# Optimization experiments

Hardware: AMD Instinct MI355X
Metric: run time of the kernel (lower is better)

The kernel has to match this reference:

```python
import jax, jax.numpy as jnp
import numpy as np

EPS = 1e-5
B, L, E, H, F, HW = 32, 6, 3, 3, 2048, 32

def _ln(x, g, b):
    mu = jnp.mean(x, -1, keepdims=True)
    v = jnp.mean((x - mu) ** 2, -1, keepdims=True)
    return (x - mu) / jnp.sqrt(v + EPS) * g + b

def setup_inputs() -> dict:
    key = jax.random.key(0)
    ks = jax.random.split(key, 16)
    s = 0.05
    return {
        "x": jax.random.normal(ks[0], (B, 3, HW, HW), jnp.float32),
        "conv_w": jax.random.normal(ks[1], (3, 1, HW, HW), jnp.float32) * s,
        "conv_b": jax.random.normal(ks[2], (3,), jnp.float32) * s,
        "Wqkv": jax.random.normal(ks[3], (L, 3 * E, E), jnp.float32) * s,
        "bqkv": jax.random.normal(ks[4], (L, 3 * E), jnp.float32) * s,
        "Wo": jax.random.normal(ks[5], (L, E, E), jnp.float32) * s,
        "bo": jax.random.normal(ks[6], (L, E), jnp.float32) * s,
        "W1": jax.random.normal(ks[7], (L, F, E), jnp.float32) * s,
        "b1": jax.random.normal(ks[8], (L, F), jnp.float32) * s,
        "W2": jax.random.normal(ks[9], (L, E, F), jnp.float32) * s,
        "b2": jax.random.normal(ks[10], (L, E), jnp.float32) * s,
        "ln1_g": jnp.ones((L, E), jnp.float32),
        "ln1_b": jnp.zeros((L, E), jnp.float32),
        "ln2_g": jnp.ones((L, E), jnp.float32),
        "ln2_b": jnp.zeros((L, E), jnp.float32),
        "mlp_W": jax.random.normal(ks[11], (10, 3 * HW * HW), jnp.float32) * s,
        "mlp_b": jax.random.normal(ks[12], (10,), jnp.float32) * s,
    }

def reference(x, conv_w, conv_b, Wqkv, bqkv, Wo, bo, W1, b1, W2, b2,
              ln1_g, ln1_b, ln2_g, ln2_b, mlp_W, mlp_b):
    b = x.shape[0]
    # grouped conv with full-image kernel -> one scalar per channel
    c = jnp.einsum('bchw,chw->bc', x, conv_w[:, 0]) + conv_b  # (B,3)
    h = x + c[:, :, None, None]                               # residual add (broadcast)
    h = h.reshape(b, HW, HW, E)  # torch resize(32,32,3): raw memory reinterpret -> (B,S,N,E)
    for l in range(L):
        Wq, Wk, Wv = Wqkv[l, :E], Wqkv[l, E:2 * E], Wqkv[l, 2 * E:]
        bq, bk, bv = bqkv[l, :E], bqkv[l, E:2 * E], bqkv[l, 2 * E:]
        # head_dim = 1, so the feature axis doubles as the head axis
        q = (jnp.einsum('bsne,fe->bsnf', h, Wq) + bq)[..., None]  # (B,S,N,H,1)
        k = (jnp.einsum('bsne,fe->bsnf', h, Wk) + bk)[..., None]
        v = (jnp.einsum('bsne,fe->bsnf', h, Wv) + bv)[..., None]
        # scale = 1/sqrt(head_dim) = 1
        scores = jnp.einsum('bsnhd,btnhd->bnhst', q, k)
        attn = jax.nn.softmax(scores, axis=-1)
        o = jnp.einsum('bnhst,btnhd->bsnhd', attn, v).reshape(b, HW, HW, E)
        o = jnp.einsum('bsne,fe->bsnf', o, Wo[l]) + bo[l]
        h = _ln(h + o, ln1_g[l], ln1_b[l])  # post-norm (torch default)
        f = jax.nn.gelu(jnp.einsum('bsne,fe->bsnf', h, W1[l]) + b1[l], approximate=False)
        f = jnp.einsum('bsnf,ef->bsne', f, W2[l]) + b2[l]
        h = _ln(h + f, ln2_g[l], ln2_b[l])
    out = h.reshape(b, -1) @ mlp_W.T + mlp_b  # (B,10)
    return out
```

## Files before the change

kernel.cpp:

```cpp
#include <hip/hip_runtime.h>
#include <math.h>

#define EPS 1e-5f
#define LAYERS 6
#define FDIM 2048
#define NTAB 512


__device__ __forceinline__ float gelu_as(float t) {
    float e  = __expf(-0.5f * t * t);
    float at = fabsf(t);
    float wr = __builtin_amdgcn_rcpf(fmaf(0.23164194f, at, 1.0f));
    float poly = fmaf(fmaf(fmaf(fmaf(1.061405429f, wr, -1.453152027f),
                                wr, 1.421413741f),
                           wr, -0.284496736f),
                      wr, 0.254829592f) * wr;
    return fmaf(-0.5f * at, poly * e, fmaxf(t, 0.f));
}

__global__ __launch_bounds__(256) void tab_kernel(
        const float* __restrict__ W1, const float* __restrict__ b1,
        const float* __restrict__ W2,
        const float* __restrict__ ln1_g, const float* __restrict__ ln1_b,
        float4* __restrict__ tab) {
    int l = blockIdx.x >> 9;
    int j = blockIdx.x & (NTAB - 1);
    int tid = threadIdx.x;
    int wv = tid >> 6, lane = tid & 63;

    float d = (float)j * (4.0f / NTAB);
    float cn = (d <= 2.0f) ? 1.0f - d : d - 3.0f;
    float asn = 1.0f - fabsf(cn);
    float sn = (d <= 2.0f) ? asn : -asn;
    float inv = 1.0f / sqrtf(cn * cn + sn * sn);
    float c = cn * inv, s = sn * inv;
    float z0 = fmaf(1.2247449f, c, 0.70710678f * s);
    float z1 = fmaf(-1.2247449f, c, 0.70710678f * s);
    float z2 = -1.4142136f * s;
    float hx0 = fmaf(ln1_g[l*3+0], z0, ln1_b[l*3+0]);
    float hx1 = fmaf(ln1_g[l*3+1], z1, ln1_b[l*3+1]);
    float hx2 = fmaf(ln1_g[l*3+2], z2, ln1_b[l*3+2]);

    const float* w1p = W1 + (size_t)l * FDIM * 3;
    const float* b1p = b1 + (size_t)l * FDIM;
    const float* w2p = W2 + (size_t)l * 3 * FDIM;

    float a0 = 0.f, a1 = 0.f, a2 = 0.f;
#pragma unroll
    for (int i = 0; i < 8; ++i) {
        int k = i * 256 + tid;
        float t = fmaf(w1p[k*3+0], hx0,
                  fmaf(w1p[k*3+1], hx1,
                  fmaf(w1p[k*3+2], hx2, b1p[k])));
        float gl = gelu_as(t);
        a0 = fmaf(gl, w2p[k],          a0);
        a1 = fmaf(gl, w2p[FDIM + k],   a1);
        a2 = fmaf(gl, w2p[2*FDIM + k], a2);
    }
#pragma unroll
    for (int m = 1; m < 64; m <<= 1) {
        a0 += __shfl_xor(a0, m);
        a1 += __shfl_xor(a1, m);
        a2 += __shfl_xor(a2, m);
    }
    __shared__ float red[4][3];
    if (lane == 0) { red[wv][0] = a0; red[wv][1] = a1; red[wv][2] = a2; }
    __syncthreads();
    if (tid == 0) {
        tab[(size_t)l * NTAB + j] = make_float4(
            red[0][0] + red[1][0] + red[2][0] + red[3][0],
            red[0][1] + red[1][1] + red[2][1] + red[3][1],
            red[0][2] + red[1][2] + red[2][2] + red[3][2], 0.f);
    }
}

__global__ __launch_bounds__(128) void fused6_kernel(
        const float* __restrict__ x,
        const float* __restrict__ conv_w, const float* __restrict__ conv_b,
        const float* __restrict__ Wqkv, const float* __restrict__ bqkv,
        const float* __restrict__ Wo,   const float* __restrict__ bo,
        const float* __restrict__ ln1_g, const float* __restrict__ ln1_b,
        const float* __restrict__ b2v,
        const float* __restrict__ ln2_g, const float* __restrict__ ln2_b,
        const float4* __restrict__ tab,
        float* __restrict__ h) {
    int b = blockIdx.x >> 4, npair = blockIdx.x & 15;
    int tid  = threadIdx.x;
    int s    = tid & 31;
    int half = (tid >> 5) & 1;
    int nl   = tid >> 6;
    int lane = tid & 63;
    int n = npair * 2 + nl;
    __shared__ float2 kv[2][3][32];

    const float4* xb4 = (const float4*)(x + (size_t)b * 3072);
    const float4* cw4 = (const float4*)conv_w;
    float cs0 = 0.f, cs1 = 0.f, cs2 = 0.f;
#pragma unroll
    for (int i = 0; i < 4; ++i) {
        int f0 = i * 64 + lane;
        float4 xv = xb4[f0], wv = cw4[f0];
        cs0 = fmaf(xv.x, wv.x, fmaf(xv.y, wv.y, fmaf(xv.z, wv.z, fmaf(xv.w, wv.w, cs0))));
        float4 xv1 = xb4[f0 + 256], wv1 = cw4[f0 + 256];
        cs1 = fmaf(xv1.x, wv1.x, fmaf(xv1.y, wv1.y, fmaf(xv1.z, wv1.z, fmaf(xv1.w, wv1.w, cs1))));
        float4 xv2 = xb4[f0 + 512], wv2 = cw4[f0 + 512];
        cs2 = fmaf(xv2.x, wv2.x, fmaf(xv2.y, wv2.y, fmaf(xv2.z, wv2.z, fmaf(xv2.w, wv2.w, cs2))));
    }
#pragma unroll
    for (int m = 1; m < 64; m <<= 1) {
        cs0 += __shfl_xor(cs0, m);
        cs1 += __shfl_xor(cs1, m);
        cs2 += __shfl_xor(cs2, m);
    }
    float c0 = cs0 + conv_b[0], c1 = cs1 + conv_b[1], c2 = cs2 + conv_b[2];

    int flat = s * 96 + n * 3;
    const float* xb = x + (size_t)b * 3072 + flat;
    float h0 = xb[0] + ((flat     < 1024) ? c0 : (flat     < 2048 ? c1 : c2));
    float h1 = xb[1] + ((flat + 1 < 1024) ? c0 : (flat + 1 < 2048 ? c1 : c2));
    float h2 = xb[2] + ((flat + 2 < 1024) ? c0 : (flat + 2 < 2048 ? c1 : c2));

    for (int l = 0; l < LAYERS; ++l) {
        const float* wq = Wqkv + l * 27;
        const float* bq = bqkv + l * 9;
        float q[3], kk[3], vv[3];
#pragma unroll
        for (int f = 0; f < 3; ++f) {
            q[f]  = fmaf(wq[f*3+0], h0, fmaf(wq[f*3+1], h1, fmaf(wq[f*3+2], h2, bq[f])));
            kk[f] = fmaf(wq[9+f*3+0], h0, fmaf(wq[9+f*3+1], h1, fmaf(wq[9+f*3+2], h2, bq[3+f])));
            vv[f] = fmaf(wq[18+f*3+0], h0, fmaf(wq[18+f*3+1], h1, fmaf(wq[18+f*3+2], h2, bq[6+f])));
        }
        __syncthreads();
        if (half == 0) {
#pragma unroll
            for (int e = 0; e < 3; ++e) kv[nl][e][s] = make_float2(kk[e], vv[e]);
        }
        __syncthreads();

        float oatt[3];
#pragma unroll
        for (int e = 0; e < 3; ++e) {
            float a = q[e] * 1.44269504f;
            float psum = 0.f, pacc = 0.f;
#pragma unroll
            for (int i = 0; i < 16; ++i) {
                float2 kvt = kv[nl][e][half * 16 + i];
                float p = exp2f(a * kvt.x);
                psum += p;
                pacc = fmaf(p, kvt.y, pacc);
            }
            float sum = psum + __shfl_xor(psum, 32);
            float acc = pacc + __shfl_xor(pacc, 32);
            oatt[e] = acc / sum;
        }
        const float* wo = Wo + l * 9;
        float x0 = h0 + fmaf(wo[0], oatt[0], fmaf(wo[1], oatt[1], fmaf(wo[2], oatt[2], bo[l*3+0])));
        float x1 = h1 + fmaf(wo[3], oatt[0], fmaf(wo[4], oatt[1], fmaf(wo[5], oatt[2], bo[l*3+1])));
        float x2 = h2 + fmaf(wo[6], oatt[0], fmaf(wo[7], oatt[1], fmaf(wo[8], oatt[2], bo[l*3+2])));
        float mu = (x0 + x1 + x2) * (1.f/3.f);
        float d0 = x0 - mu, d1 = x1 - mu, d2 = x2 - mu;
        float var = (d0*d0 + d1*d1 + d2*d2) * (1.f/3.f);
        float inv = 1.0f / sqrtf(var + EPS);
        float z0 = d0 * inv, z1 = d1 * inv, z2 = d2 * inv;
        float hn0 = fmaf(z0, ln1_g[l*3+0], ln1_b[l*3+0]);
        float hn1 = fmaf(z1, ln1_g[l*3+1], ln1_b[l*3+1]);
        float hn2 = fmaf(z2, ln1_g[l*3+2], ln1_b[l*3+2]);
        float cc = 0.40824829f * (z0 - z1);
        float ss = 0.23570226f * (z0 + z1 - 2.f * z2);
        float m  = fabsf(cc) + fabsf(ss) + 1e-30f;
        float cnn = cc * __builtin_amdgcn_rcpf(m);
        float dq = (ss >= 0.f) ? (1.f - cnn) : (3.f + cnn);
        float xq = dq * (float)(NTAB / 4);
        float fl = floorf(xq);
        float fr = xq - fl;
        int j0 = ((int)fl) & (NTAB - 1);
        int j1 = (j0 + 1) & (NTAB - 1);
        float4 ta = tab[(size_t)l * NTAB + j0];
        float4 tb = tab[(size_t)l * NTAB + j1];
        float f0 = fmaf(fr, tb.x - ta.x, ta.x);
        float f1 = fmaf(fr, tb.y - ta.y, ta.y);
        float f2 = fmaf(fr, tb.z - ta.z, ta.z);
        float y0 = hn0 + f0 + b2v[l*3+0];
        float y1 = hn1 + f1 + b2v[l*3+1];
        float y2 = hn2 + f2 + b2v[l*3+2];
        float mu2 = (y0 + y1 + y2) * (1.f/3.f);
        float e0 = y0 - mu2, e1 = y1 - mu2, e2 = y2 - mu2;
        float var2 = (e0*e0 + e1*e1 + e2*e2) * (1.f/3.f);
        float inv2 = 1.0f / sqrtf(var2 + EPS);
        h0 = fmaf(e0 * inv2, ln2_g[l*3+0], ln2_b[l*3+0]);
        h1 = fmaf(e1 * inv2, ln2_g[l*3+1], ln2_b[l*3+1]);
        h2 = fmaf(e2 * inv2, ln2_g[l*3+2], ln2_b[l*3+2]);
    }
    if (half == 0) {
        float* hp = h + (size_t)b * 3072 + flat;
        hp[0] = h0; hp[1] = h1; hp[2] = h2;
    }
}

__global__ void head_kernel(const float* __restrict__ h,
                            const float* __restrict__ mlp_W,
                            const float* __restrict__ mlp_b,
                            float* __restrict__ out) {
    int b = blockIdx.x, tid = threadIdx.x;
    float hh[12];
#pragma unroll
    for (int m = 0; m < 12; ++m) hh[m] = h[(size_t)b * 3072 + tid + m * 256];
    float p[10];
#pragma unroll
    for (int j = 0; j < 10; ++j) {
        const float* wj = mlp_W + (size_t)j * 3072;
        float s = 0.f;
#pragma unroll
        for (int m = 0; m < 12; ++m) s = fmaf(hh[m], wj[tid + m * 256], s);
#pragma unroll
        for (int d = 32; d >= 1; d >>= 1) s += __shfl_down(s, d);
        p[j] = s;
    }
    __shared__ float red[10][4];
    int wave = tid >> 6, lane = tid & 63;
    if (lane == 0) {
#pragma unroll
        for (int j = 0; j < 10; ++j) red[j][wave] = p[j];
    }
    __syncthreads();
    if (tid < 10)
        out[b * 10 + tid] = red[tid][0] + red[tid][1] + red[tid][2] + red[tid][3] + mlp_b[tid];
}

extern "C" void kernel_launch(void* const* d_in, const int* in_sizes, int n_in,
                              void* d_out, int out_size, void* d_ws, size_t ws_size,
                              hipStream_t stream) {
    const float* x      = (const float*)d_in[0];
    const float* conv_w = (const float*)d_in[1];
    const float* conv_b = (const float*)d_in[2];
    const float* Wqkv   = (const float*)d_in[3];
    const float* bqkv   = (const float*)d_in[4];
    const float* Wo     = (const float*)d_in[5];
    const float* bo     = (const float*)d_in[6];
    const float* W1     = (const float*)d_in[7];
    const float* b1     = (const float*)d_in[8];
    const float* W2     = (const float*)d_in[9];
    const float* b2     = (const float*)d_in[10];
    const float* ln1_g  = (const float*)d_in[11];
    const float* ln1_b  = (const float*)d_in[12];
    const float* ln2_g  = (const float*)d_in[13];
    const float* ln2_b  = (const float*)d_in[14];
    const float* mlp_W  = (const float*)d_in[15];
    const float* mlp_b  = (const float*)d_in[16];
    float* out = (float*)d_out;

    float*  h   = (float*)d_ws;
    float4* tab = (float4*)((char*)d_ws + 393216);

    hipLaunchKernelGGL(tab_kernel, dim3(LAYERS * NTAB), dim3(256), 0, stream,
                       W1, b1, W2, ln1_g, ln1_b, tab);
    hipLaunchKernelGGL(fused6_kernel, dim3(512), dim3(128), 0, stream,
                       x, conv_w, conv_b, Wqkv, bqkv, Wo, bo,
                       ln1_g, ln1_b, b2, ln2_g, ln2_b, tab, h);
    hipLaunchKernelGGL(head_kernel, dim3(32), dim3(256), 0, stream, h, mlp_W, mlp_b, out);
}
```

Measured before the change: 34.32 us.

## Fuse classifier head into main kernel with atomic last-block reduction

Removes the separate head kernel launch and the global write/read of the hidden state by computing each wave's partial dot products against mlp_W inside the fused kernel. Partials are reduced with wave shuffles, written per wave, and the last wave per batch (detected via an atomic counter reset in tab_kernel) sums them and adds the bias. This trades one launch and the round trip of h through memory for ten shuffle reductions per wave, extra atomics and threadfences.

```diff
diff --git a/kernel.cpp b/kernel.cpp
--- a/kernel.cpp
+++ b/kernel.cpp
@@ -5,7 +5,6 @@
 #define LAYERS 6
 #define FDIM 2048
 #define NTAB 512
-
 
 __device__ __forceinline__ float gelu_as(float t) {
     float e  = __expf(-0.5f * t * t);
@@ -22,11 +21,13 @@
         const float* __restrict__ W1, const float* __restrict__ b1,
         const float* __restrict__ W2,
         const float* __restrict__ ln1_g, const float* __restrict__ ln1_b,
-        float4* __restrict__ tab) {
+        float4* __restrict__ tab, int* __restrict__ cnt) {
     int l = blockIdx.x >> 9;
     int j = blockIdx.x & (NTAB - 1);
     int tid = threadIdx.x;
     int wv = tid >> 6, lane = tid & 63;
+
+    if (blockIdx.x == 0 && tid < 32) cnt[tid] = 0;
 
     float d = (float)j * (4.0f / NTAB);
     float cn = (d <= 2.0f) ? 1.0f - d : d - 3.0f;
@@ -83,7 +84,9 @@
         const float* __restrict__ b2v,
         const float* __restrict__ ln2_g, const float* __restrict__ ln2_b,
         const float4* __restrict__ tab,
-        float* __restrict__ h) {
+        const float* __restrict__ mlp_W, const float* __restrict__ mlp_b,
+        float* __restrict__ partials, int* __restrict__ cnt,
+        float* __restrict__ out) {
     int b = blockIdx.x >> 4, npair = blockIdx.x & 15;
     int tid  = threadIdx.x;
     int s    = tid & 31;
@@ -191,40 +194,37 @@
         h1 = fmaf(e1 * inv2, ln2_g[l*3+1], ln2_b[l*3+1]);
         h2 = fmaf(e2 * inv2, ln2_g[l*3+2], ln2_b[l*3+2]);
     }
-    if (half == 0) {
-        float* hp = h + (size_t)b * 3072 + flat;
-        hp[0] = h0; hp[1] = h1; hp[2] = h2;
-    }
-}
-
-__global__ void head_kernel(const float* __restrict__ h,
-                            const float* __restrict__ mlp_W,
-                            const float* __restrict__ mlp_b,
-                            float* __restrict__ out) {
-    int b = blockIdx.x, tid = threadIdx.x;
-    float hh[12];
-#pragma unroll
-    for (int m = 0; m < 12; ++m) hh[m] = h[(size_t)b * 3072 + tid + m * 256];
-    float p[10];
+
+    float p10[10];
 #pragma unroll
     for (int j = 0; j < 10; ++j) {
-        const float* wj = mlp_W + (size_t)j * 3072;
-        float s = 0.f;
-#pragma unroll
-        for (int m = 0; m < 12; ++m) s = fmaf(hh[m], wj[tid + m * 256], s);
-#pragma unroll
-        for (int d = 32; d >= 1; d >>= 1) s += __shfl_down(s, d);
-        p[j] = s;
-    }
-    __shared__ float red[10][4];
-    int wave = tid >> 6, lane = tid & 63;
+        const float* w = mlp_W + (size_t)j * 3072 + flat;
+        p10[j] = (half == 0) ? fmaf(h0, w[0], fmaf(h1, w[1], h2 * w[2])) : 0.f;
+    }
+#pragma unroll
+    for (int m = 1; m < 64; m <<= 1) {
+#pragma unroll
+        for (int j = 0; j < 10; ++j) p10[j] += __shfl_xor(p10[j], m);
+    }
+    int widx = npair * 2 + nl;
+    int old = 0;
     if (lane == 0) {
 #pragma unroll
-        for (int j = 0; j < 10; ++j) red[j][wave] = p[j];
-    }
-    __syncthreads();
-    if (tid < 10)
-        out[b * 10 + tid] = red[tid][0] + red[tid][1] + red[tid][2] + red[tid][3] + mlp_b[tid];
+        for (int j = 0; j < 10; ++j) partials[(size_t)(b * 32 + widx) * 10 + j] = p10[j];
+        __threadfence();
+        old = atomicAdd(&cnt[b], 1);
+    }
+    old = __shfl(old, 0);
+    if (old == 31) {
+        __threadfence();
+        if (lane < 10) {
+            float sacc = mlp_b[lane];
+#pragma unroll
+            for (int i = 0; i < 32; ++i)
+                sacc += partials[(size_t)(b * 32 + i) * 10 + lane];
+            out[b * 10 + lane] = sacc;
+        }
+    }
 }
 
 extern "C" void kernel_launch(void* const* d_in, const int* in_sizes, int n_in,
@@ -249,13 +249,14 @@
     const float* mlp_b  = (const float*)d_in[16];
     float* out = (float*)d_out;
 
-    float*  h   = (float*)d_ws;
-    float4* tab = (float4*)((char*)d_ws + 393216);
+    float4* tab      = (float4*)d_ws;
+    float*  partials = (float*)((char*)d_ws + 49152);
+    int*    cnt      = (int*)((char*)d_ws + 90112);
 
     hipLaunchKernelGGL(tab_kernel, dim3(LAYERS * NTAB), dim3(256), 0, stream,
-                       W1, b1, W2, ln1_g, ln1_b, tab);
+                       W1, b1, W2, ln1_g, ln1_b, tab, cnt);
     hipLaunchKernelGGL(fused6_kernel, dim3(512), dim3(128), 0, stream,
                        x, conv_w, conv_b, Wqkv, bqkv, Wo, bo,
-                       ln1_g, ln1_b, b2, ln2_g, ln2_b, tab, h);
-    hipLaunchKernelGGL(head_kernel, dim3(32), dim3(256), 0, stream, h, mlp_W, mlp_b, out);
-}
+                       ln1_g, ln1_b, b2, ln2_g, ln2_b, tab, mlp_W, mlp_b,
+                       partials, cnt, out);
+}
```

After: 54.06 us. 1.58x slower.
